# Kernel tuning notes

Hardware: AMD Instinct MI355X
Metric: run time of the kernel (lower is better)

## Reference

```python
import jax, jax.numpy as jnp
import numpy as np

N, F_IN, F_OUT, K = 4096, 32, 32, 2
NEG_SLOPE = 0.2
MASK_VAL = -9e15


def _sparse_mat(kv, km, density=0.01):
    vals = jax.random.normal(kv, (N, N), dtype=jnp.float32)
    mask = jax.random.uniform(km, (N, N)) < density
    return vals * mask


def setup_inputs() -> dict:
    key = jax.random.key(0)
    ks = jax.random.split(key, 12)
    x = jax.random.normal(ks[0], (N, F_IN), dtype=jnp.float32)
    Ld = _sparse_mat(ks[1], ks[2])
    Lu = _sparse_mat(ks[3], ks[4])
    P = jax.random.normal(ks[5], (N, N), dtype=jnp.float32) / np.sqrt(N)
    W1 = jax.random.normal(ks[6], (K, F_IN, F_OUT), dtype=jnp.float32) * 0.1
    W2 = jax.random.normal(ks[7], (K, F_IN, F_OUT), dtype=jnp.float32) * 0.1
    W0 = jax.random.normal(ks[8], (F_IN, F_OUT), dtype=jnp.float32) * 0.1
    att1 = jax.random.normal(ks[9], (2 * F_OUT * K, 1), dtype=jnp.float32) * 0.1
    att2 = jax.random.normal(ks[10], (2 * F_OUT * K, 1), dtype=jnp.float32) * 0.1
    return {"x": x, "Ld": Ld, "Lu": Lu, "P": P, "W1": W1, "W2": W2,
            "W0": W0, "att1": att1, "att2": att2}


def _branch(x, L, W, att):
    # W: [K, F_in, F_out]; precompute x @ W[k] for all k -> [K, N, F_out]
    Kk, _, Fo = W.shape
    xw = jnp.einsum('nf,kfo->kno', x, W)
    # torch.cat([x@W[k]], dim=1) == transpose+reshape of xw
    xcat = jnp.transpose(xw, (1, 0, 2)).reshape(x.shape[0], Kk * Fo)
    d = Fo * Kk
    e = xcat @ att[:d] + (xcat @ att[d:]).T            # [N, N]
    e = jax.nn.leaky_relu(e, negative_slope=NEG_SLOPE)
    e = jnp.where(L != 0, e, MASK_VAL)
    alpha = jax.nn.softmax(e, axis=1)                   # row softmax, no dropout (eval)
    z = alpha @ xw[0]
    a = alpha
    for k in range(1, Kk):
        a = a @ L
        z = z + a @ xw[k]
    return z


def reference(x, Ld, Lu, P, W1, W2, W0, att1, att2):
    z1 = _branch(x, Ld, W1, att1)
    z2 = _branch(x, Lu, W2, att2)
    x0 = P @ (x @ W0)
    return z1 + z2 + x0
```

## Files before the change

kernel.cpp:

```cpp
#include <hip/hip_runtime.h>
#include <hip/hip_bf16.h>

#define NN 4096
#define CAP 128
#define KS 8

typedef __attribute__((ext_vector_type(8))) short bf16x8;
typedef __attribute__((ext_vector_type(4))) float f32x4;

__device__ __forceinline__ float lrelu(float v) { return v >= 0.f ? v : 0.2f * v; }

__device__ __forceinline__ ushort f2bu(float f) {
    unsigned u = __float_as_uint(f);
    return (ushort)((u + 0x7FFFu + ((u >> 16) & 1u)) >> 16);
}

__global__ __launch_bounds__(256) void k_prep(
    const float* __restrict__ x,
    const float* __restrict__ W1, const float* __restrict__ W2,
    const float* __restrict__ W0,
    const float* __restrict__ att1, const float* __restrict__ att2,
    float* __restrict__ xwA1, float* __restrict__ xwB1,
    float* __restrict__ xwA2, float* __restrict__ xwB2,
    float* __restrict__ a1, float* __restrict__ b1,
    float* __restrict__ a2, float* __restrict__ b2,
    __hip_bfloat16* __restrict__ Bt)
{
    __shared__ float wl[5120];
    __shared__ float xs[256];
    const int t = threadIdx.x;
    for (int i = t; i < 2048; i += 256) { wl[i] = W1[i]; wl[2048 + i] = W2[i]; }
    for (int i = t; i < 1024; i += 256) wl[4096 + i] = W0[i];
    const int rowBase = blockIdx.x * 8;
    xs[t] = x[rowBase * 32 + t];
    __syncthreads();

    const int o = t & 31, r = t >> 5;
    const int row = rowBase + r;
    const float* xr = &xs[r * 32];
    float vA1 = 0.f, vB1 = 0.f, vA2 = 0.f, vB2 = 0.f, v0 = 0.f;
#pragma unroll
    for (int f = 0; f < 32; ++f) {
        const float xv = xr[f];
        vA1 += xv * wl[f * 32 + o];
        vB1 += xv * wl[1024 + f * 32 + o];
        vA2 += xv * wl[2048 + f * 32 + o];
        vB2 += xv * wl[3072 + f * 32 + o];
        v0  += xv * wl[4096 + f * 32 + o];
    }
    xwA1[row * 32 + o] = vA1;
    xwB1[row * 32 + o] = vB1;
    xwA2[row * 32 + o] = vA2;
    xwB2[row * 32 + o] = vB2;
    ((ushort*)Bt)[(size_t)o * NN + row] = f2bu(v0);

    float pa1 = vA1 * att1[o]      + vB1 * att1[32 + o];
    float pb1 = vA1 * att1[64 + o] + vB1 * att1[96 + o];
    float pa2 = vA2 * att2[o]      + vB2 * att2[32 + o];
    float pb2 = vA2 * att2[64 + o] + vB2 * att2[96 + o];
#pragma unroll
    for (int m = 1; m <= 16; m <<= 1) {
        pa1 += __shfl_xor(pa1, m); pb1 += __shfl_xor(pb1, m);
        pa2 += __shfl_xor(pa2, m); pb2 += __shfl_xor(pb2, m);
    }
    if (o == 0) { a1[row] = pa1; b1[row] = pb1; a2[row] = pa2; b2[row] = pb2; }
}

__global__ __launch_bounds__(256) void k_work(
    const float* __restrict__ Ld, const float* __restrict__ Lu,
    const float* __restrict__ P, const ushort* __restrict__ Bt,
    int2* __restrict__ csrv, int* __restrict__ cntArr,
    float* __restrict__ partial)
{
    __shared__ ushort sA[16 * 64 * 8];
    __shared__ ushort sB[8 * 64 * 8];
    const int t = threadIdx.x;
    const int lane = t & 63, w = t >> 6;
    const int bx = blockIdx.x;

    if (bx % 9 == 0) {
        const int bp = bx / 9;
        const int row0 = (bp & 63) * 64;
        const int ks = bp >> 6;
        const float4*  P4  = (const float4*)P;
        const ushort4* Bt4 = (const ushort4*)Bt;
        f32x4 acc0 = {0.f, 0.f, 0.f, 0.f};
        f32x4 acc1 = {0.f, 0.f, 0.f, 0.f};

        for (int c = 0; c < 4; ++c) {
            const int kc4 = (ks * 512 + c * 128) >> 2;
#pragma unroll
            for (int j = 0; j < 8; ++j) {
                const int i = t + 256 * j;
                const int row = i >> 5, q = i & 31;
                const float4 v = P4[(size_t)(row0 + row) * 1024 + kc4 + q];
                ushort4 u;
                u.x = f2bu(v.x); u.y = f2bu(v.y); u.z = f2bu(v.z); u.w = f2bu(v.w);
                const int wi = row >> 4, m = row & 15;
                const int kk = q >> 3, quad = (q >> 1) & 3, jj = q & 1;
                *(ushort4*)&sA[(((wi * 4 + kk) * 64) + quad * 16 + m) * 8 + jj * 4] = u;
            }
#pragma unroll
            for (int j = 0; j < 4; ++j) {
                const int i = t + 256 * j;
                const int o = i >> 5, q = i & 31;
                const ushort4 u = Bt4[(size_t)o * 1024 + kc4 + q];
                const int nt = o >> 4, n = o & 15;
                const int kk = q >> 3, quad = (q >> 1) & 3, jj = q & 1;
                *(ushort4*)&sB[(((kk * 2 + nt) * 64) + quad * 16 + n) * 8 + jj * 4] = u;
            }
            __syncthreads();
            const ushort* pa = &sA[(w * 4) * 64 * 8 + lane * 8];
            const ushort* pb = &sB[lane * 8];
#pragma unroll
            for (int kk = 0; kk < 4; ++kk) {
                const bf16x8 a  = *(const bf16x8*)(pa + kk * 512);
                const bf16x8 b0 = *(const bf16x8*)(pb + kk * 1024);
                const bf16x8 b1 = *(const bf16x8*)(pb + kk * 1024 + 512);
                acc0 = __builtin_amdgcn_mfma_f32_16x16x32_bf16(a, b0, acc0, 0, 0, 0);
                acc1 = __builtin_amdgcn_mfma_f32_16x16x32_bf16(a, b1, acc1, 0, 0, 0);
            }
            __syncthreads();
        }
        const int m = lane & 15, quad = lane >> 4;
        float* out = partial + ((size_t)ks * NN + row0 + w * 16 + quad * 4) * 32;
#pragma unroll
        for (int r = 0; r < 4; ++r) {
            out[r * 32 + m]      = acc0[r];
            out[r * 32 + 16 + m] = acc1[r];
        }
    } else {
        const int row = bx - 1 - bx / 9;
        int* wcnt = (int*)sA;

        float4 v[8];
        const float4* A4 = (const float4*)(Ld + (size_t)row * NN);
        const float4* B4 = (const float4*)(Lu + (size_t)row * NN);
#pragma unroll
        for (int it = 0; it < 4; ++it) { v[it] = A4[it * 256 + t]; v[4 + it] = B4[it * 256 + t]; }

        const unsigned long long lt = (1ull << lane) - 1ull;
#pragma unroll
        for (int br = 0; br < 2; ++br) {
            int2* out = csrv + ((size_t)br * NN + row) * CAP;
            int tots[4];
#pragma unroll
            for (int it = 0; it < 4; ++it) {
                const float4 fv = v[br * 4 + it];
                tots[it] = __popcll(__ballot(fv.x != 0.f)) + __popcll(__ballot(fv.y != 0.f))
                         + __popcll(__ballot(fv.z != 0.f)) + __popcll(__ballot(fv.w != 0.f));
            }
            __syncthreads();
            if (lane == 0) {
                int4 tv; tv.x = tots[0]; tv.y = tots[1]; tv.z = tots[2]; tv.w = tots[3];
                *(int4*)&wcnt[w * 4] = tv;
            }
            __syncthreads();
            const int4 ca = *(const int4*)&wcnt[0];
            const int4 cb = *(const int4*)&wcnt[4];
            const int4 cc = *(const int4*)&wcnt[8];
            const int4 cd = *(const int4*)&wcnt[12];
            const int cs[16] = {ca.x, ca.y, ca.z, ca.w, cb.x, cb.y, cb.z, cb.w,
                                cc.x, cc.y, cc.z, cc.w, cd.x, cd.y, cd.z, cd.w};
            int total = 0;
#pragma unroll
            for (int k2 = 0; k2 < 16; ++k2) total += cs[k2];
            int base = 0;
#pragma unroll
            for (int k2 = 0; k2 < 16; ++k2) base += (k2 < (w << 2)) ? cs[k2] : 0;
            const int cnt  = min(total, CAP);
            const int cp16 = min((cnt + 15) & ~15, CAP);

#pragma unroll
            for (int it = 0; it < 4; ++it) {
                const float4 fv = v[br * 4 + it];
                const unsigned long long m0 = __ballot(fv.x != 0.f);
                const unsigned long long m1 = __ballot(fv.y != 0.f);
                const unsigned long long m2 = __ballot(fv.z != 0.f);
                const unsigned long long m3 = __ballot(fv.w != 0.f);
                const int p0 = __popcll(m0), p1 = __popcll(m1), p2 = __popcll(m2);
                const int c0 = (it * 256 + t) * 4;
                int s;
                s = base + __popcll(m0 & lt);
                if (fv.x != 0.f && s < CAP) { int2 e; e.x = c0;     e.y = __float_as_int(fv.x); out[s] = e; }
                s = base + p0 + __popcll(m1 & lt);
                if (fv.y != 0.f && s < CAP) { int2 e; e.x = c0 + 1; e.y = __float_as_int(fv.y); out[s] = e; }
                s = base + p0 + p1 + __popcll(m2 & lt);
                if (fv.z != 0.f && s < CAP) { int2 e; e.x = c0 + 2; e.y = __float_as_int(fv.z); out[s] = e; }
                s = base + p0 + p1 + p2 + __popcll(m3 & lt);
                if (fv.w != 0.f && s < CAP) { int2 e; e.x = c0 + 3; e.y = __float_as_int(fv.w); out[s] = e; }
                base += p0 + p1 + p2 + __popcll(m3);
            }
            if (t >= cnt && t < cp16) { int2 e; e.x = 0; e.y = 0; out[t] = e; }
            if (t == 0) cntArr[br * NN + row] = cnt;
        }
    }
}

__global__ __launch_bounds__(256) void k_gather(
    const int2* __restrict__ csrv, const int* __restrict__ cntArr,
    const float* __restrict__ xwB1, const float* __restrict__ xwB2,
    const float* __restrict__ xwA1, const float* __restrict__ xwA2,
    float* __restrict__ u1, float* __restrict__ u2)
{
    __shared__ int2 sle[4][CAP];
    const int w = threadIdx.x >> 6, lane = threadIdx.x & 63;
    const int row = blockIdx.x * 4 + w;
    const int br  = blockIdx.y;
    const float* xwB = br ? xwB2 : xwB1;
    const float* xwA = br ? xwA2 : xwA1;
    float* u = br ? u2 : u1;

    const int cnt  = cntArr[br * NN + row];
    const int cp16 = min((cnt + 15) & ~15, CAP);
    const int2* ci = csrv + ((size_t)br * NN + row) * CAP;
    int2* se = sle[w];
    if (lane < cp16)      se[lane]      = ci[lane];
    if (lane + 64 < cp16) se[lane + 64] = ci[lane + 64];

    const int o = lane & 31, g = lane >> 5;
    float acc = 0.f;
    const int nb = cp16 >> 3;
    for (int j = 0; j < nb; ++j) {
        float wv[4], xv[4];
#pragma unroll
        for (int q = 0; q < 4; ++q) {
            const int2 e = se[8 * j + 2 * q + g];
            wv[q] = __int_as_float(e.y);
            xv[q] = xwB[(size_t)e.x * 32 + o];
        }
#pragma unroll
        for (int q = 0; q < 4; ++q) acc += wv[q] * xv[q];
    }
    acc += __shfl_xor(acc, 32);
    if (lane < 32) u[(size_t)row * 32 + o] = acc + xwA[(size_t)row * 32 + o];
}

__global__ __launch_bounds__(256) void k_attn2(
    const int2* __restrict__ csrv, const int* __restrict__ cntArr,
    const float* __restrict__ a1, const float* __restrict__ b1,
    const float* __restrict__ a2, const float* __restrict__ b2,
    const float* __restrict__ u1, const float* __restrict__ u2,
    const float* __restrict__ partial, float* __restrict__ outp)
{
    __shared__ float sw[4 * CAP];
    __shared__ int   sci[4 * CAP];
    const int w = threadIdx.x >> 6, lane = threadIdx.x & 63;
    const int row = blockIdx.x * 4 + w;
    float* swg = sw + w * CAP;
    int*   scg = sci + w * CAP;
    const int o = lane & 31, h = lane >> 5;
    float total = 0.f;

#pragma unroll
    for (int br = 0; br < 2; ++br) {
        const float* aA = br ? a2 : a1;
        const float* bA = br ? b2 : b1;
        const float* U  = br ? u2 : u1;
        const int cnt = cntArr[br * NN + row];
        const int cp16 = min((cnt + 15) & ~15, CAP);
        const float ai = aA[row];
        const int2* ci = csrv + ((size_t)br * NN + row) * CAP;

        int id0 = 0, id1 = 0;
        if (lane < cp16)      id0 = ci[lane].x;
        if (lane + 64 < cp16) id1 = ci[lane + 64].x;
        float e0 = (lane < cnt)      ? lrelu(ai + bA[id0]) : -1e30f;
        float e1 = (lane + 64 < cnt) ? lrelu(ai + bA[id1]) : -1e30f;
        float lmax = fmaxf(e0, e1);
#pragma unroll
        for (int m = 1; m <= 32; m <<= 1) lmax = fmaxf(lmax, __shfl_xor(lmax, m));
        const float w0 = __expf(e0 - lmax), w1 = __expf(e1 - lmax);
        float ssum = w0 + w1;
#pragma unroll
        for (int m = 1; m <= 32; m <<= 1) ssum += __shfl_xor(ssum, m);
        swg[lane] = w0; swg[lane + 64] = w1;
        scg[lane] = id0; scg[lane + 64] = id1;

        float acc = 0.f;
        const int nb = cp16 >> 3;
        if (cnt > 0) {
            float wgA[4], uvA[4];
#pragma unroll
            for (int q = 0; q < 4; ++q) {
                const int s = h + 2 * q;
                wgA[q] = swg[s];
                uvA[q] = U[(size_t)scg[s] * 32 + o];
            }
            for (int j = 1; j < nb; ++j) {
                float wgB[4], uvB[4];
#pragma unroll
                for (int q = 0; q < 4; ++q) {
                    const int s = h + 8 * j + 2 * q;
                    wgB[q] = swg[s];
                    uvB[q] = U[(size_t)scg[s] * 32 + o];
                }
#pragma unroll
                for (int q = 0; q < 4; ++q) acc += wgA[q] * uvA[q];
#pragma unroll
                for (int q = 0; q < 4; ++q) { wgA[q] = wgB[q]; uvA[q] = uvB[q]; }
            }
#pragma unroll
            for (int q = 0; q < 4; ++q) acc += wgA[q] * uvA[q];
        }
        acc += __shfl_xor(acc, 32);
        if (cnt > 0) total += acc / ssum;
    }

    if (lane < 32) {
#pragma unroll
        for (int p = 0; p < KS; ++p)
            total += partial[(size_t)p * NN * 32 + (size_t)row * 32 + o];
        outp[(size_t)row * 32 + o] = total;
    }
}

extern "C" void kernel_launch(void* const* d_in, const int* in_sizes, int n_in,
                              void* d_out, int out_size, void* d_ws, size_t ws_size,
                              hipStream_t stream) {
    (void)in_sizes; (void)n_in; (void)out_size; (void)ws_size;
    const float* x    = (const float*)d_in[0];
    const float* Ld   = (const float*)d_in[1];
    const float* Lu   = (const float*)d_in[2];
    const float* P    = (const float*)d_in[3];
    const float* W1   = (const float*)d_in[4];
    const float* W2   = (const float*)d_in[5];
    const float* W0   = (const float*)d_in[6];
    const float* att1 = (const float*)d_in[7];
    const float* att2 = (const float*)d_in[8];

    float* ws = (float*)d_ws;
    float* xwA1 = ws;
    float* xwB1 = ws + 131072;
    float* xwA2 = ws + 262144;
    float* xwB2 = ws + 393216;
    float* u1   = ws + 524288;
    float* u2   = ws + 655360;
    float* a1   = ws + 786432;
    float* b1   = ws + 790528;
    float* a2   = ws + 794624;
    float* b2   = ws + 798720;
    float* partial = ws + 802816;
    __hip_bfloat16* Bt = (__hip_bfloat16*)(ws + 1851392);
    int2* csrv = (int2*)(ws + 1916928);
    int*  cnt  = (int*)(ws + 4014080);

    k_prep<<<512, 256, 0, stream>>>(x, W1, W2, W0, att1, att2,
                                    xwA1, xwB1, xwA2, xwB2, a1, b1, a2, b2, Bt);
    k_work<<<4608, 256, 0, stream>>>(Ld, Lu, P, (const ushort*)Bt,
                                     csrv, cnt, partial);
    k_gather<<<dim3(NN / 4, 2), 256, 0, stream>>>(csrv, cnt, xwB1, xwB2,
                                                  xwA1, xwA2, u1, u2);
    k_attn2<<<NN / 4, 256, 0, stream>>>(csrv, cnt, a1, b1, a2, b2,
                                        u1, u2, partial, (float*)d_out);
}
```

Before: 243.3 us.

## Split fused CSR/GEMM kernel, move softmax into gather, double-buffer P GEMM

Splits the interleaved k_work kernel into a CSR-building kernel that handles two rows per block and a separate P@(xW0) GEMM kernel with double-buffered shared memory. The attention softmax weights are computed once in the gather kernel and written back normalized into the CSR value slots, so the final kernel only performs weighted gathers and the partial-sum reduction. The aim is to remove redundant softmax work and uneven mixed-block scheduling. In exchange it adds a kernel launch, overwrites the CSR values in place, and serializes the CSR build and the GEMM as separate kernels.

```diff
diff --git a/kernel.cpp b/kernel.cpp
--- a/kernel.cpp
+++ b/kernel.cpp
@@ -66,141 +66,94 @@
     if (o == 0) { a1[row] = pa1; b1[row] = pb1; a2[row] = pa2; b2[row] = pb2; }
 }
 
-__global__ __launch_bounds__(256) void k_work(
+__global__ __launch_bounds__(256) void k_csr2(
     const float* __restrict__ Ld, const float* __restrict__ Lu,
-    const float* __restrict__ P, const ushort* __restrict__ Bt,
-    int2* __restrict__ csrv, int* __restrict__ cntArr,
-    float* __restrict__ partial)
-{
-    __shared__ ushort sA[16 * 64 * 8];
-    __shared__ ushort sB[8 * 64 * 8];
-    const int t = threadIdx.x;
-    const int lane = t & 63, w = t >> 6;
-    const int bx = blockIdx.x;
-
-    if (bx % 9 == 0) {
-        const int bp = bx / 9;
-        const int row0 = (bp & 63) * 64;
-        const int ks = bp >> 6;
-        const float4*  P4  = (const float4*)P;
-        const ushort4* Bt4 = (const ushort4*)Bt;
-        f32x4 acc0 = {0.f, 0.f, 0.f, 0.f};
-        f32x4 acc1 = {0.f, 0.f, 0.f, 0.f};
-
-        for (int c = 0; c < 4; ++c) {
-            const int kc4 = (ks * 512 + c * 128) >> 2;
-#pragma unroll
-            for (int j = 0; j < 8; ++j) {
-                const int i = t + 256 * j;
-                const int row = i >> 5, q = i & 31;
-                const float4 v = P4[(size_t)(row0 + row) * 1024 + kc4 + q];
-                ushort4 u;
-                u.x = f2bu(v.x); u.y = f2bu(v.y); u.z = f2bu(v.z); u.w = f2bu(v.w);
-                const int wi = row >> 4, m = row & 15;
-                const int kk = q >> 3, quad = (q >> 1) & 3, jj = q & 1;
-                *(ushort4*)&sA[(((wi * 4 + kk) * 64) + quad * 16 + m) * 8 + jj * 4] = u;
-            }
-#pragma unroll
-            for (int j = 0; j < 4; ++j) {
-                const int i = t + 256 * j;
-                const int o = i >> 5, q = i & 31;
-                const ushort4 u = Bt4[(size_t)o * 1024 + kc4 + q];
-                const int nt = o >> 4, n = o & 15;
-                const int kk = q >> 3, quad = (q >> 1) & 3, jj = q & 1;
-                *(ushort4*)&sB[(((kk * 2 + nt) * 64) + quad * 16 + n) * 8 + jj * 4] = u;
-            }
-            __syncthreads();
-            const ushort* pa = &sA[(w * 4) * 64 * 8 + lane * 8];
-            const ushort* pb = &sB[lane * 8];
-#pragma unroll
-            for (int kk = 0; kk < 4; ++kk) {
-                const bf16x8 a  = *(const bf16x8*)(pa + kk * 512);
-                const bf16x8 b0 = *(const bf16x8*)(pb + kk * 1024);
-                const bf16x8 b1 = *(const bf16x8*)(pb + kk * 1024 + 512);
-                acc0 = __builtin_amdgcn_mfma_f32_16x16x32_bf16(a, b0, acc0, 0, 0, 0);
-                acc1 = __builtin_amdgcn_mfma_f32_16x16x32_bf16(a, b1, acc1, 0, 0, 0);
-            }
-            __syncthreads();
-        }
-        const int m = lane & 15, quad = lane >> 4;
-        float* out = partial + ((size_t)ks * NN + row0 + w * 16 + quad * 4) * 32;
-#pragma unroll
-        for (int r = 0; r < 4; ++r) {
-            out[r * 32 + m]      = acc0[r];
-            out[r * 32 + 16 + m] = acc1[r];
-        }
-    } else {
-        const int row = bx - 1 - bx / 9;
-        int* wcnt = (int*)sA;
-
-        float4 v[8];
-        const float4* A4 = (const float4*)(Ld + (size_t)row * NN);
-        const float4* B4 = (const float4*)(Lu + (size_t)row * NN);
-#pragma unroll
-        for (int it = 0; it < 4; ++it) { v[it] = A4[it * 256 + t]; v[4 + it] = B4[it * 256 + t]; }
-
-        const unsigned long long lt = (1ull << lane) - 1ull;
-#pragma unroll
-        for (int br = 0; br < 2; ++br) {
-            int2* out = csrv + ((size_t)br * NN + row) * CAP;
-            int tots[4];
-#pragma unroll
-            for (int it = 0; it < 4; ++it) {
-                const float4 fv = v[br * 4 + it];
-                tots[it] = __popcll(__ballot(fv.x != 0.f)) + __popcll(__ballot(fv.y != 0.f))
-                         + __popcll(__ballot(fv.z != 0.f)) + __popcll(__ballot(fv.w != 0.f));
-            }
-            __syncthreads();
-            if (lane == 0) {
-                int4 tv; tv.x = tots[0]; tv.y = tots[1]; tv.z = tots[2]; tv.w = tots[3];
-                *(int4*)&wcnt[w * 4] = tv;
-            }
-            __syncthreads();
-            const int4 ca = *(const int4*)&wcnt[0];
-            const int4 cb = *(const int4*)&wcnt[4];
-            const int4 cc = *(const int4*)&wcnt[8];
-            const int4 cd = *(const int4*)&wcnt[12];
-            const int cs[16] = {ca.x, ca.y, ca.z, ca.w, cb.x, cb.y, cb.z, cb.w,
-                                cc.x, cc.y, cc.z, cc.w, cd.x, cd.y, cd.z, cd.w};
-            int total = 0;
-#pragma unroll
-            for (int k2 = 0; k2 < 16; ++k2) total += cs[k2];
-            int base = 0;
-#pragma unroll
-            for (int k2 = 0; k2 < 16; ++k2) base += (k2 < (w << 2)) ? cs[k2] : 0;
-            const int cnt  = min(total, CAP);
-            const int cp16 = min((cnt + 15) & ~15, CAP);
-
-#pragma unroll
-            for (int it = 0; it < 4; ++it) {
-                const float4 fv = v[br * 4 + it];
-                const unsigned long long m0 = __ballot(fv.x != 0.f);
-                const unsigned long long m1 = __ballot(fv.y != 0.f);
-                const unsigned long long m2 = __ballot(fv.z != 0.f);
-                const unsigned long long m3 = __ballot(fv.w != 0.f);
-                const int p0 = __popcll(m0), p1 = __popcll(m1), p2 = __popcll(m2);
-                const int c0 = (it * 256 + t) * 4;
-                int s;
-                s = base + __popcll(m0 & lt);
-                if (fv.x != 0.f && s < CAP) { int2 e; e.x = c0;     e.y = __float_as_int(fv.x); out[s] = e; }
-                s = base + p0 + __popcll(m1 & lt);
-                if (fv.y != 0.f && s < CAP) { int2 e; e.x = c0 + 1; e.y = __float_as_int(fv.y); out[s] = e; }
-                s = base + p0 + p1 + __popcll(m2 & lt);
-                if (fv.z != 0.f && s < CAP) { int2 e; e.x = c0 + 2; e.y = __float_as_int(fv.z); out[s] = e; }
-                s = base + p0 + p1 + p2 + __popcll(m3 & lt);
-                if (fv.w != 0.f && s < CAP) { int2 e; e.x = c0 + 3; e.y = __float_as_int(fv.w); out[s] = e; }
-                base += p0 + p1 + p2 + __popcll(m3);
-            }
-            if (t >= cnt && t < cp16) { int2 e; e.x = 0; e.y = 0; out[t] = e; }
-            if (t == 0) cntArr[br * NN + row] = cnt;
-        }
-    }
-}
-
-__global__ __launch_bounds__(256) void k_gather(
-    const int2* __restrict__ csrv, const int* __restrict__ cntArr,
+    int2* __restrict__ csrv, int* __restrict__ cntArr)
+{
+    const int r0 = blockIdx.x * 2;
+    const int t = threadIdx.x, lane = t & 63, w = t >> 6;
+    __shared__ int wcnt[16];
+
+    float4 v[16];
+    {
+        const float4* A0 = (const float4*)(Ld + (size_t)r0 * NN);
+        const float4* B0 = (const float4*)(Lu + (size_t)r0 * NN);
+        const float4* A1 = (const float4*)(Ld + (size_t)(r0 + 1) * NN);
+        const float4* B1 = (const float4*)(Lu + (size_t)(r0 + 1) * NN);
+#pragma unroll
+        for (int it = 0; it < 4; ++it) {
+            v[it]      = A0[it * 256 + t];
+            v[4 + it]  = B0[it * 256 + t];
+            v[8 + it]  = A1[it * 256 + t];
+            v[12 + it] = B1[it * 256 + t];
+        }
+    }
+
+    const unsigned long long lt = (1ull << lane) - 1ull;
+#pragma unroll
+    for (int c = 0; c < 4; ++c) {
+        const int row = r0 + (c >> 1);
+        const int br  = c & 1;
+        int2* out = csrv + ((size_t)br * NN + row) * CAP;
+        int tots[4];
+#pragma unroll
+        for (int it = 0; it < 4; ++it) {
+            const float4 fv = v[c * 4 + it];
+            tots[it] = __popcll(__ballot(fv.x != 0.f)) + __popcll(__ballot(fv.y != 0.f))
+                     + __popcll(__ballot(fv.z != 0.f)) + __popcll(__ballot(fv.w != 0.f));
+        }
+        __syncthreads();
+        if (lane == 0) {
+            int4 tv; tv.x = tots[0]; tv.y = tots[1]; tv.z = tots[2]; tv.w = tots[3];
+            *(int4*)&wcnt[w * 4] = tv;
+        }
+        __syncthreads();
+        const int4 ca = *(const int4*)&wcnt[0];
+        const int4 cb = *(const int4*)&wcnt[4];
+        const int4 cc = *(const int4*)&wcnt[8];
+        const int4 cd = *(const int4*)&wcnt[12];
+        const int cs[16] = {ca.x, ca.y, ca.z, ca.w, cb.x, cb.y, cb.z, cb.w,
+                            cc.x, cc.y, cc.z, cc.w, cd.x, cd.y, cd.z, cd.w};
+        int total = 0;
+#pragma unroll
+        for (int k2 = 0; k2 < 16; ++k2) total += cs[k2];
+        int base = 0;
+#pragma unroll
+        for (int k2 = 0; k2 < 16; ++k2) base += (k2 < (w << 2)) ? cs[k2] : 0;
+        const int cnt  = min(total, CAP);
+        const int cp16 = min((cnt + 15) & ~15, CAP);
+
+#pragma unroll
+        for (int it = 0; it < 4; ++it) {
+            const float4 fv = v[c * 4 + it];
+            const unsigned long long m0 = __ballot(fv.x != 0.f);
+            const unsigned long long m1 = __ballot(fv.y != 0.f);
+            const unsigned long long m2 = __ballot(fv.z != 0.f);
+            const unsigned long long m3 = __ballot(fv.w != 0.f);
+            const int p0 = __popcll(m0), p1 = __popcll(m1), p2 = __popcll(m2);
+            const int c0 = (it * 256 + t) * 4;
+            int s;
+            s = base + __popcll(m0 & lt);
+            if (fv.x != 0.f && s < CAP) { int2 e; e.x = c0;     e.y = __float_as_int(fv.x); out[s] = e; }
+            s = base + p0 + __popcll(m1 & lt);
+            if (fv.y != 0.f && s < CAP) { int2 e; e.x = c0 + 1; e.y = __float_as_int(fv.y); out[s] = e; }
+            s = base + p0 + p1 + __popcll(m2 & lt);
+            if (fv.z != 0.f && s < CAP) { int2 e; e.x = c0 + 2; e.y = __float_as_int(fv.z); out[s] = e; }
+            s = base + p0 + p1 + p2 + __popcll(m3 & lt);
+            if (fv.w != 0.f && s < CAP) { int2 e; e.x = c0 + 3; e.y = __float_as_int(fv.w); out[s] = e; }
+            base += p0 + p1 + p2 + __popcll(m3);
+        }
+        if (t >= cnt && t < cp16) { int2 e; e.x = 0; e.y = 0; out[t] = e; }
+        if (t == 0) cntArr[br * NN + row] = cnt;
+    }
+}
+
+__global__ __launch_bounds__(256) void k_gather2(
+    int2* __restrict__ csrv, const int* __restrict__ cntArr,
     const float* __restrict__ xwB1, const float* __restrict__ xwB2,
     const float* __restrict__ xwA1, const float* __restrict__ xwA2,
+    const float* __restrict__ a1, const float* __restrict__ b1,
+    const float* __restrict__ a2, const float* __restrict__ b2,
     float* __restrict__ u1, float* __restrict__ u2)
 {
     __shared__ int2 sle[4][CAP];
@@ -209,14 +162,31 @@
     const int br  = blockIdx.y;
     const float* xwB = br ? xwB2 : xwB1;
     const float* xwA = br ? xwA2 : xwA1;
+    const float* aA  = br ? a2 : a1;
+    const float* bA  = br ? b2 : b1;
     float* u = br ? u2 : u1;
 
     const int cnt  = cntArr[br * NN + row];
     const int cp16 = min((cnt + 15) & ~15, CAP);
-    const int2* ci = csrv + ((size_t)br * NN + row) * CAP;
+    int2* ci = csrv + ((size_t)br * NN + row) * CAP;
     int2* se = sle[w];
-    if (lane < cp16)      se[lane]      = ci[lane];
-    if (lane + 64 < cp16) se[lane + 64] = ci[lane + 64];
+    int2 l0 = {0, 0}, l1 = {0, 0};
+    if (lane < cp16)      { l0 = ci[lane];      se[lane]      = l0; }
+    if (lane + 64 < cp16) { l1 = ci[lane + 64]; se[lane + 64] = l1; }
+
+    const float ai = aA[row];
+    const float e0 = (lane < cnt)      ? lrelu(ai + bA[l0.x]) : -1e30f;
+    const float e1 = (lane + 64 < cnt) ? lrelu(ai + bA[l1.x]) : -1e30f;
+    float lmax = fmaxf(e0, e1);
+#pragma unroll
+    for (int m = 1; m <= 32; m <<= 1) lmax = fmaxf(lmax, __shfl_xor(lmax, m));
+    const float w0 = __expf(e0 - lmax), w1 = __expf(e1 - lmax);
+    float ssum = w0 + w1;
+#pragma unroll
+    for (int m = 1; m <= 32; m <<= 1) ssum += __shfl_xor(ssum, m);
+    const float inv = (cnt > 0) ? 1.f / ssum : 0.f;
+    if (lane < cp16)      { l0.y = __float_as_int((lane < cnt)      ? w0 * inv : 0.f); ci[lane]      = l0; }
+    if (lane + 64 < cp16) { l1.y = __float_as_int((lane + 64 < cnt) ? w1 * inv : 0.f); ci[lane + 64] = l1; }
 
     const int o = lane & 31, g = lane >> 5;
     float acc = 0.f;
@@ -236,75 +206,46 @@
     if (lane < 32) u[(size_t)row * 32 + o] = acc + xwA[(size_t)row * 32 + o];
 }
 
-__global__ __launch_bounds__(256) void k_attn2(
+__global__ __launch_bounds__(256) void k_accum(
     const int2* __restrict__ csrv, const int* __restrict__ cntArr,
-    const float* __restrict__ a1, const float* __restrict__ b1,
-    const float* __restrict__ a2, const float* __restrict__ b2,
     const float* __restrict__ u1, const float* __restrict__ u2,
     const float* __restrict__ partial, float* __restrict__ outp)
 {
-    __shared__ float sw[4 * CAP];
-    __shared__ int   sci[4 * CAP];
+    __shared__ int2 sle[4][2 * CAP];
     const int w = threadIdx.x >> 6, lane = threadIdx.x & 63;
     const int row = blockIdx.x * 4 + w;
-    float* swg = sw + w * CAP;
-    int*   scg = sci + w * CAP;
-    const int o = lane & 31, h = lane >> 5;
+    const int o = lane & 31, g = lane >> 5;
+    int2* se = sle[w];
     float total = 0.f;
 
+    int cp[2];
 #pragma unroll
     for (int br = 0; br < 2; ++br) {
-        const float* aA = br ? a2 : a1;
-        const float* bA = br ? b2 : b1;
-        const float* U  = br ? u2 : u1;
         const int cnt = cntArr[br * NN + row];
-        const int cp16 = min((cnt + 15) & ~15, CAP);
-        const float ai = aA[row];
+        cp[br] = min((cnt + 15) & ~15, CAP);
         const int2* ci = csrv + ((size_t)br * NN + row) * CAP;
-
-        int id0 = 0, id1 = 0;
-        if (lane < cp16)      id0 = ci[lane].x;
-        if (lane + 64 < cp16) id1 = ci[lane + 64].x;
-        float e0 = (lane < cnt)      ? lrelu(ai + bA[id0]) : -1e30f;
-        float e1 = (lane + 64 < cnt) ? lrelu(ai + bA[id1]) : -1e30f;
-        float lmax = fmaxf(e0, e1);
-#pragma unroll
-        for (int m = 1; m <= 32; m <<= 1) lmax = fmaxf(lmax, __shfl_xor(lmax, m));
-        const float w0 = __expf(e0 - lmax), w1 = __expf(e1 - lmax);
-        float ssum = w0 + w1;
-#pragma unroll
-        for (int m = 1; m <= 32; m <<= 1) ssum += __shfl_xor(ssum, m);
-        swg[lane] = w0; swg[lane + 64] = w1;
-        scg[lane] = id0; scg[lane + 64] = id1;
-
+        if (lane < cp[br])      se[br * CAP + lane]      = ci[lane];
+        if (lane + 64 < cp[br]) se[br * CAP + lane + 64] = ci[lane + 64];
+    }
+
+#pragma unroll
+    for (int br = 0; br < 2; ++br) {
+        const float* U = br ? u2 : u1;
         float acc = 0.f;
-        const int nb = cp16 >> 3;
-        if (cnt > 0) {
-            float wgA[4], uvA[4];
+        const int nb = cp[br] >> 3;
+        for (int j = 0; j < nb; ++j) {
+            float wv[4], uv[4];
 #pragma unroll
             for (int q = 0; q < 4; ++q) {
-                const int s = h + 2 * q;
-                wgA[q] = swg[s];
-                uvA[q] = U[(size_t)scg[s] * 32 + o];
+                const int2 e = se[br * CAP + 8 * j + 2 * q + g];
+                wv[q] = __int_as_float(e.y);
+                uv[q] = U[(size_t)e.x * 32 + o];
             }
-            for (int j = 1; j < nb; ++j) {
-                float wgB[4], uvB[4];
-#pragma unroll
-                for (int q = 0; q < 4; ++q) {
-                    const int s = h + 8 * j + 2 * q;
-                    wgB[q] = swg[s];
-                    uvB[q] = U[(size_t)scg[s] * 32 + o];
-                }
-#pragma unroll
-                for (int q = 0; q < 4; ++q) acc += wgA[q] * uvA[q];
-#pragma unroll
-                for (int q = 0; q < 4; ++q) { wgA[q] = wgB[q]; uvA[q] = uvB[q]; }
-            }
-#pragma unroll
-            for (int q = 0; q < 4; ++q) acc += wgA[q] * uvA[q];
+#pragma unroll
+            for (int q = 0; q < 4; ++q) acc += wv[q] * uv[q];
         }
         acc += __shfl_xor(acc, 32);
-        if (cnt > 0) total += acc / ssum;
+        total += acc;
     }
 
     if (lane < 32) {
@@ -312,6 +253,79 @@
         for (int p = 0; p < KS; ++p)
             total += partial[(size_t)p * NN * 32 + (size_t)row * 32 + o];
         outp[(size_t)row * 32 + o] = total;
+    }
+}
+
+__global__ __launch_bounds__(256) void k_pgemm(
+    const float* __restrict__ P, const ushort* __restrict__ Bt,
+    float* __restrict__ partial)
+{
+    __shared__ ushort sA[2][16 * 64 * 8];
+    __shared__ ushort sB[2][8 * 64 * 8];
+    const int t = threadIdx.x;
+    const int row0 = blockIdx.x * 64;
+    const int ks = blockIdx.y;
+    const float4*  P4  = (const float4*)P;
+    const ushort4* Bt4 = (const ushort4*)Bt;
+
+    const int lane = t & 63, w = t >> 6;
+
+    f32x4 acc0 = {0.f, 0.f, 0.f, 0.f};
+    f32x4 acc1 = {0.f, 0.f, 0.f, 0.f};
+
+    auto stageA = [&](int c, int buf) {
+        const int kc4 = (ks * 512 + c * 128) >> 2;
+#pragma unroll
+        for (int j = 0; j < 8; ++j) {
+            const int i = t + 256 * j;
+            const int row = i >> 5, q = i & 31;
+            const float4 v = P4[(size_t)(row0 + row) * 1024 + kc4 + q];
+            ushort4 u;
+            u.x = f2bu(v.x); u.y = f2bu(v.y); u.z = f2bu(v.z); u.w = f2bu(v.w);
+            const int wi = row >> 4, m = row & 15;
+            const int kk = q >> 3, quad = (q >> 1) & 3, jj = q & 1;
+            *(ushort4*)&sA[buf][(((wi * 4 + kk) * 64) + quad * 16 + m) * 8 + jj * 4] = u;
+        }
+    };
+    auto stageB = [&](int c, int buf) {
+        const int kc4 = (ks * 512 + c * 128) >> 2;
+#pragma unroll
+        for (int j = 0; j < 4; ++j) {
+            const int i = t + 256 * j;
+            const int o = i >> 5, q = i & 31;
+            const ushort4 u = Bt4[(size_t)o * 1024 + kc4 + q];
+            const int nt = o >> 4, n = o & 15;
+            const int kk = q >> 3, quad = (q >> 1) & 3, jj = q & 1;
+            *(ushort4*)&sB[buf][(((kk * 2 + nt) * 64) + quad * 16 + n) * 8 + jj * 4] = u;
+        }
+    };
+    auto compute = [&](int buf) {
+        const ushort* pa = &sA[buf][(w * 4) * 64 * 8 + lane * 8];
+        const ushort* pb = &sB[buf][lane * 8];
+#pragma unroll
+        for (int kk = 0; kk < 4; ++kk) {
+            const bf16x8 a  = *(const bf16x8*)(pa + kk * 512);
+            const bf16x8 b0 = *(const bf16x8*)(pb + kk * 1024);
+            const bf16x8 b1 = *(const bf16x8*)(pb + kk * 1024 + 512);
+            acc0 = __builtin_amdgcn_mfma_f32_16x16x32_bf16(a, b0, acc0, 0, 0, 0);
+            acc1 = __builtin_amdgcn_mfma_f32_16x16x32_bf16(a, b1, acc1, 0, 0, 0);
+        }
+    };
+
+    stageA(0, 0); stageB(0, 0);
+    __syncthreads();
+    for (int c = 0; c < 4; ++c) {
+        if (c < 3) { stageA(c + 1, (c + 1) & 1); stageB(c + 1, (c + 1) & 1); }
+        compute(c & 1);
+        __syncthreads();
+    }
+
+    const int m = lane & 15, quad = lane >> 4;
+    float* out = partial + ((size_t)ks * NN + row0 + w * 16 + quad * 4) * 32;
+#pragma unroll
+    for (int r = 0; r < 4; ++r) {
+        out[r * 32 + m]      = acc0[r];
+        out[r * 32 + 16 + m] = acc1[r];
     }
 }
 
@@ -347,10 +361,11 @@
 
     k_prep<<<512, 256, 0, stream>>>(x, W1, W2, W0, att1, att2,
                                     xwA1, xwB1, xwA2, xwB2, a1, b1, a2, b2, Bt);
-    k_work<<<4608, 256, 0, stream>>>(Ld, Lu, P, (const ushort*)Bt,
-                                     csrv, cnt, partial);
-    k_gather<<<dim3(NN / 4, 2), 256, 0, stream>>>(csrv, cnt, xwB1, xwB2,
-                                                  xwA1, xwA2, u1, u2);
-    k_attn2<<<NN / 4, 256, 0, stream>>>(csrv, cnt, a1, b1, a2, b2,
-                                        u1, u2, partial, (float*)d_out);
-}
+    k_csr2<<<NN / 2, 256, 0, stream>>>(Ld, Lu, csrv, cnt);
+    k_pgemm<<<dim3(64, KS), 256, 0, stream>>>(P, (const ushort*)Bt, partial);
+    k_gather2<<<dim3(NN / 4, 2), 256, 0, stream>>>(csrv, cnt, xwB1, xwB2,
+                                                   xwA1, xwA2, a1, b1, a2, b2,
+                                                   u1, u2);
+    k_accum<<<NN / 4, 256, 0, stream>>>(csrv, cnt, u1, u2, partial,
+                                        (float*)d_out);
+}
```

After: 236.9 us. 2.6% less time.
